# Kernel optimization log

Measured on AMD Instinct MI355X. Metric: run time of the kernel, lower is better.

## Reference

```python
import jax, jax.numpy as jnp
import numpy as np

N = 512          # nodes per sample (num_nodes)
B = 8            # batch size (samples)
H = 64           # hidden_dim
SPARSITY = 0.1
K = int(SPARSITY * N * (N - 1))  # edges kept per sample (fixed, static)


def setup_inputs() -> dict:
    key = jax.random.key(0)
    ks = jax.random.split(key, 8)

    def lin(k, fi, fo):
        w = jax.random.normal(k, (fi, fo), jnp.float32) / np.sqrt(fi).astype(np.float32)
        b = jnp.zeros((fo,), jnp.float32)
        return w, b

    w_emb, b_emb = lin(ks[0], 1, H)
    w_proj, b_proj = lin(ks[1], H, H)
    w1, b1 = lin(ks[2], 2 * H, H)
    w2, b2 = lin(ks[3], H, H // 2)
    w3, b3 = lin(ks[4], H // 2, 1)
    x = jax.random.uniform(ks[5], (B * N, 1), jnp.float32)  # abundances >= 0
    batch = jnp.repeat(jnp.arange(B, dtype=jnp.int32), N)   # [B*N]
    return dict(x=x, w_emb=w_emb, b_emb=b_emb, w_proj=w_proj, b_proj=b_proj,
                w1=w1, b1=b1, w2=w2, b2=b2, w3=w3, b3=b3, batch=batch)


def reference(x, w_emb, b_emb, w_proj, b_proj, w1, b1, w2, b2, w3, b3, batch):
    # node embedding + projection (dropout is eval-mode no-op)
    emb = jax.nn.relu(x @ w_emb + b_emb) @ w_proj + b_proj     # [B*N, H]
    emb = emb.reshape(B, N, H)
    # first pairwise-MLP layer: cat([e_i, e_j]) @ w1 == e_i @ w1a + e_j @ w1b
    w1a, w1b = w1[:H], w1[H:]
    ai = emb @ w1a                                            # [B, N, H]
    aj = emb @ w1b                                            # [B, N, H]
    h1 = jax.nn.relu(ai[:, :, None, :] + aj[:, None, :, :] + b1)   # [B, N, N, H]
    h2 = jax.nn.relu(jnp.einsum('bijh,hk->bijk', h1, w2) + b2)     # [B, N, N, H/2]
    probs = jax.nn.sigmoid(jnp.einsum('bijk,ko->bij', h2, w3) + b3[0])  # [B, N, N]
    probs = 0.5 * (probs + jnp.swapaxes(probs, 1, 2))          # symmetrize
    probs = probs * (1.0 - jnp.eye(N, dtype=probs.dtype))      # mask diagonal
    flat = probs.reshape(B, N * N)
    _, idx = jax.lax.top_k(flat, K)                            # [B, K]
    idx = jnp.sort(idx, axis=-1)                               # row-major order (dense_to_sparse)
    vals = jnp.take_along_axis(flat, idx, axis=-1)             # [B, K]
    offsets = (jnp.arange(B) * N)[:, None]                     # node offset per sample
    rows = idx // N + offsets
    cols = idx % N + offsets
    edge_index = jnp.stack([rows.reshape(-1), cols.reshape(-1)], axis=0)  # [2, B*K]
    edge_weights = vals.reshape(-1)                            # [B*K]
    adj = jnp.zeros((B, N * N), flat.dtype).at[jnp.arange(B)[:, None], idx].set(vals)
    adj = adj.reshape(B, N, N)                                 # sparse adjacency per sample
    return edge_index, edge_weights, adj
```

## Files before the change

kernel.cpp:

```cpp
#include <hip/hip_runtime.h>

#define NV 512
#define BV 8
#define HV 64
#define KSEL 26163
#define NNv (NV*NV)
#define BKv (BV*KSEL)

typedef unsigned int u32;
typedef __attribute__((ext_vector_type(2))) float f32x2;

__global__ void k_init(u32* __restrict__ hist4, u32* __restrict__ prefix,
                       u32* __restrict__ remK) {
    const int t = blockIdx.x * 256 + threadIdx.x;
    if (t < 8192) hist4[t] = 0u;
    if (t < 8) { prefix[t] = 0u; remK[t] = (u32)KSEL; }
}

__global__ void __launch_bounds__(256) k_embed(
    const float* __restrict__ x, const float* __restrict__ w_emb,
    const float* __restrict__ b_emb, const float* __restrict__ w_proj,
    const float* __restrict__ b_proj, const float* __restrict__ w1,
    float* __restrict__ ai, float* __restrict__ aj) {
    __shared__ float sh[4][64];
    __shared__ float se[4][64];
    const int c = threadIdx.x;
    const int lr = threadIdx.y;
    const int row = blockIdx.x * 4 + lr;
    const float xv = x[row];
    sh[lr][c] = fmaxf(fmaf(xv, w_emb[c], b_emb[c]), 0.f);
    __syncthreads();
    float e = 0.f;
#pragma unroll
    for (int h = 0; h < 64; ++h) e = fmaf(sh[lr][h], w_proj[h * 64 + c], e);
    se[lr][c] = e + b_proj[c];
    __syncthreads();
    float a0 = 0.f, a1 = 0.f;
#pragma unroll
    for (int h = 0; h < 64; ++h) {
        const float ev = se[lr][h];
        a0 = fmaf(ev, w1[h * 64 + c], a0);
        a1 = fmaf(ev, w1[(64 + h) * 64 + c], a1);
    }
    ai[row * 64 + c] = a0;
    aj[row * 64 + c] = a1;
}

#define F4(v, c) (((const float*)&(v))[c])
__global__ void __launch_bounds__(256, 2) k_pairs(
    const float* __restrict__ ai, const float* __restrict__ aj,
    const float* __restrict__ b1, const float* __restrict__ w2,
    const float* __restrict__ b2, const float* __restrict__ w3,
    const float* __restrict__ b3, float* __restrict__ probs) {
    __shared__ float s_ai[16 * 68];
    __shared__ float s_aj[64 * 68];
    __shared__ float s_b1[64];
    __shared__ float s_w2[64 * 32];
    __shared__ float s_b2[32];
    __shared__ float s_w3[32];
    __shared__ float s_b3v;
    const int tid = threadIdx.x;
    const int b  = blockIdx.z;
    const int i0 = blockIdx.y << 4;
    const int j0 = blockIdx.x << 6;

    {
        const int r  = tid >> 4;
        const int q4 = (tid & 15) << 2;
        *(float4*)&s_ai[r * 68 + q4] =
            *(const float4*)&ai[(((b << 9) + i0 + r) << 6) + q4];
#pragma unroll
        for (int s = 0; s < 4; ++s) {
            *(float4*)&s_aj[(r + 16 * s) * 68 + q4] =
                *(const float4*)&aj[(((b << 9) + j0 + 16 * s + r) << 6) + q4];
        }
        *(float4*)&s_w2[tid * 4]        = *(const float4*)&w2[tid * 4];
        *(float4*)&s_w2[1024 + tid * 4] = *(const float4*)&w2[1024 + tid * 4];
        if (tid < 64) s_b1[tid] = b1[tid];
        if (tid < 32) { s_b2[tid] = b2[tid]; s_w3[tid] = w3[tid]; }
        if (tid == 0) s_b3v = b3[0];
    }
    __syncthreads();

    const int tj = tid & 15;
    const int ti = tid >> 4;

    f32x2 acc0[16], acc1[16], acc2[16], acc3[16];
#pragma unroll
    for (int k = 0; k < 16; ++k) {
        acc0[k] = (f32x2){0.f, 0.f}; acc1[k] = (f32x2){0.f, 0.f};
        acc2[k] = (f32x2){0.f, 0.f}; acc3[k] = (f32x2){0.f, 0.f};
    }

#pragma unroll 1
    for (int h4 = 0; h4 < 64; h4 += 4) {
        const float4 aiv = *(const float4*)&s_ai[ti * 68 + h4];
        const float4 aj0 = *(const float4*)&s_aj[(tj     ) * 68 + h4];
        const float4 aj1 = *(const float4*)&s_aj[(tj + 16) * 68 + h4];
        const float4 aj2 = *(const float4*)&s_aj[(tj + 32) * 68 + h4];
        const float4 aj3 = *(const float4*)&s_aj[(tj + 48) * 68 + h4];
        const float4 b1v = *(const float4*)&s_b1[h4];
#pragma unroll
        for (int hh = 0; hh < 4; ++hh) {
            const float ah = F4(aiv, hh);
            const float bh = F4(b1v, hh);
            const float t0 = fmaxf((ah + F4(aj0, hh)) + bh, 0.f);
            const float t1 = fmaxf((ah + F4(aj1, hh)) + bh, 0.f);
            const float t2 = fmaxf((ah + F4(aj2, hh)) + bh, 0.f);
            const float t3 = fmaxf((ah + F4(aj3, hh)) + bh, 0.f);
            const f32x2 tt0 = {t0, t0};
            const f32x2 tt1 = {t1, t1};
            const f32x2 tt2 = {t2, t2};
            const f32x2 tt3 = {t3, t3};
            const float4* w4p = (const float4*)&s_w2[(h4 + hh) << 5];
            f32x2 w2r[16];
#pragma unroll
            for (int q = 0; q < 8; ++q) {
                const float4 w = w4p[q];
                w2r[2 * q]     = (f32x2){w.x, w.y};
                w2r[2 * q + 1] = (f32x2){w.z, w.w};
            }
#pragma unroll
            for (int k = 0; k < 16; ++k) {
                asm("v_pk_fma_f32 %0, %1, %2, %0" : "+v"(acc0[k]) : "v"(w2r[k]), "v"(tt0));
                asm("v_pk_fma_f32 %0, %1, %2, %0" : "+v"(acc1[k]) : "v"(w2r[k]), "v"(tt1));
                asm("v_pk_fma_f32 %0, %1, %2, %0" : "+v"(acc2[k]) : "v"(w2r[k]), "v"(tt2));
                asm("v_pk_fma_f32 %0, %1, %2, %0" : "+v"(acc3[k]) : "v"(w2r[k]), "v"(tt3));
            }
        }
    }

    float d0 = 0.f, d1 = 0.f, d2 = 0.f, d3 = 0.f;
#pragma unroll
    for (int k = 0; k < 32; ++k) {
        const float bk = s_b2[k], wk = s_w3[k];
        d0 = fmaf(fmaxf(acc0[k >> 1][k & 1] + bk, 0.f), wk, d0);
        d1 = fmaf(fmaxf(acc1[k >> 1][k & 1] + bk, 0.f), wk, d1);
        d2 = fmaf(fmaxf(acc2[k >> 1][k & 1] + bk, 0.f), wk, d2);
        d3 = fmaf(fmaxf(acc3[k >> 1][k & 1] + bk, 0.f), wk, d3);
    }
    const float bb = s_b3v;
    const float p0 = 1.f / (1.f + expf(-(d0 + bb)));
    const float p1 = 1.f / (1.f + expf(-(d1 + bb)));
    const float p2 = 1.f / (1.f + expf(-(d2 + bb)));
    const float p3 = 1.f / (1.f + expf(-(d3 + bb)));
    const int base = (((b << 9) + i0 + ti) << 9) + j0 + tj;
    probs[base]      = p0;
    probs[base + 16] = p1;
    probs[base + 32] = p2;
    probs[base + 48] = p3;
}

__global__ void k_sym(float* __restrict__ P) {
    const int b = blockIdx.y;
    int rem = blockIdx.x, ta = 0;
    while (rem >= 16 - ta) { rem -= 16 - ta; ++ta; }
    const int tb = ta + rem;
    const int r  = threadIdx.x >> 3;
    const int c4 = (threadIdx.x & 7) << 2;
    const int i = (ta << 5) + r;
    const int j = (tb << 5) + c4;
    float* Pb = P + b * NNv;
    float4 a = *(const float4*)&Pb[(i << 9) + j];
    float t0 = Pb[((j + 0) << 9) + i];
    float t1 = Pb[((j + 1) << 9) + i];
    float t2 = Pb[((j + 2) << 9) + i];
    float t3 = Pb[((j + 3) << 9) + i];
    __syncthreads();
    float4 o;
    o.x = (i == j + 0) ? 0.f : 0.5f * (a.x + t0);
    o.y = (i == j + 1) ? 0.f : 0.5f * (a.y + t1);
    o.z = (i == j + 2) ? 0.f : 0.5f * (a.z + t2);
    o.w = (i == j + 3) ? 0.f : 0.5f * (a.w + t3);
    *(float4*)&Pb[(i << 9) + j] = o;
    Pb[((j + 0) << 9) + i] = o.x;
    Pb[((j + 1) << 9) + i] = o.y;
    Pb[((j + 2) << 9) + i] = o.z;
    Pb[((j + 3) << 9) + i] = o.w;
}

template <int P>
__global__ void k_hist(const float* __restrict__ probs,
                       const u32* __restrict__ prefix, u32* __restrict__ hist) {
    __shared__ u32 lh[1024];
    const int t = threadIdx.x;
    lh[t] = 0u; lh[256 + t] = 0u; lh[512 + t] = 0u; lh[768 + t] = 0u;
    __syncthreads();
    const int b = blockIdx.y;
    u32 pref = 0u;
    if constexpr (P > 0) pref = prefix[b];
    const float* Pb = probs + b * NNv;
    const int base = blockIdx.x * 4096 + t;
    const int rep = (t & 3) << 8;
#pragma unroll
    for (int e = 0; e < 16; ++e) {
        const u32 key = __float_as_uint(Pb[base + e * 256]);
        bool ok = true;
        if constexpr (P > 0) ok = ((key >> (32 - 8 * P)) == pref);
        if (ok) atomicAdd(&lh[rep + ((key >> (24 - 8 * P)) & 255u)], 1u);
    }
    __syncthreads();
    const u32 sum = lh[t] + lh[256 + t] + lh[512 + t] + lh[768 + t];
    if (sum) atomicAdd(&hist[b * 256 + t], sum);
}

__global__ void k_sel(const u32* __restrict__ hist, u32* __restrict__ prefix,
                      u32* __restrict__ remK) {
    __shared__ u32 s[256];
    __shared__ int cstar;
    const int b = blockIdx.x, t = threadIdx.x;
    const u32 h = hist[b * 256 + t];
    s[t] = h;
    if (t == 0) cstar = 0;
    __syncthreads();
    for (int off = 1; off < 256; off <<= 1) {
        const u32 v = (t + off < 256) ? s[t + off] : 0u;
        __syncthreads();
        s[t] += v;
        __syncthreads();
    }
    const u32 rem = remK[b];
    if (s[t] >= rem) atomicMax(&cstar, t);
    __syncthreads();
    if (t == cstar) {
        const u32 above = (t < 255) ? s[t + 1] : 0u;
        remK[b] = rem - above;
        prefix[b] = (prefix[b] << 8) | (u32)t;
    }
}

__global__ void k_count(const float* __restrict__ P, const u32* __restrict__ Tk,
                        u32* __restrict__ bgt, u32* __restrict__ beq) {
    __shared__ u32 sg[256], se[256];
    const int b = blockIdx.y, blk = blockIdx.x, t = threadIdx.x;
    const u32 T = Tk[b];
    const float4 v = *(const float4*)&P[b * NNv + blk * 1024 + t * 4];
    const u32 k0 = __float_as_uint(v.x), k1 = __float_as_uint(v.y);
    const u32 k2 = __float_as_uint(v.z), k3 = __float_as_uint(v.w);
    sg[t] = (u32)(k0 > T) + (k1 > T) + (k2 > T) + (k3 > T);
    se[t] = (u32)(k0 == T) + (k1 == T) + (k2 == T) + (k3 == T);
    __syncthreads();
    for (int s = 128; s > 0; s >>= 1) {
        if (t < s) { sg[t] += sg[t + s]; se[t] += se[t + s]; }
        __syncthreads();
    }
    if (t == 0) { bgt[b * 256 + blk] = sg[0]; beq[b * 256 + blk] = se[0]; }
}

__global__ void k_scan(const u32* __restrict__ bgt, const u32* __restrict__ beq,
                       u32* __restrict__ goff, u32* __restrict__ eoff) {
    __shared__ u32 sg[256], se[256];
    const int b = blockIdx.x, t = threadIdx.x;
    const u32 g = bgt[b * 256 + t], e = beq[b * 256 + t];
    sg[t] = g; se[t] = e;
    __syncthreads();
    for (int off = 1; off < 256; off <<= 1) {
        const u32 ag = (t >= off) ? sg[t - off] : 0u;
        const u32 ae = (t >= off) ? se[t - off] : 0u;
        __syncthreads();
        sg[t] += ag; se[t] += ae;
        __syncthreads();
    }
    goff[b * 256 + t] = sg[t] - g;
    eoff[b * 256 + t] = se[t] - e;
}

__global__ void k_write(const float* __restrict__ P, const u32* __restrict__ Tk,
                        const u32* __restrict__ Rk, const u32* __restrict__ goff,
                        const u32* __restrict__ eoff, float* __restrict__ out) {
    __shared__ u32 sg[256], se[256];
    const int b = blockIdx.y, blk = blockIdx.x, t = threadIdx.x;
    const u32 T = Tk[b];
    const u32 R = Rk[b];
    const int pbase = b * NNv;
    const int fi0 = blk * 1024 + t * 4;
    const float4 v = *(const float4*)&P[pbase + fi0];
    float vv[4] = {v.x, v.y, v.z, v.w};
    u32 kk[4];
#pragma unroll
    for (int q = 0; q < 4; ++q) kk[q] = __float_as_uint(vv[q]);
    u32 gt = 0, eq = 0;
#pragma unroll
    for (int q = 0; q < 4; ++q) { gt += (kk[q] > T); eq += (kk[q] == T); }
    sg[t] = gt; se[t] = eq;
    __syncthreads();
    for (int off = 1; off < 256; off <<= 1) {
        const u32 ag = (t >= off) ? sg[t - off] : 0u;
        const u32 ae = (t >= off) ? se[t - off] : 0u;
        __syncthreads();
        sg[t] += ag; se[t] += ae;
        __syncthreads();
    }
    u32 gt_before = goff[b * 256 + blk] + sg[t] - gt;
    u32 eq_before = eoff[b * 256 + blk] + se[t] - eq;
#pragma unroll
    for (int q = 0; q < 4; ++q) {
        const u32 key = kk[q];
        const float val = vv[q];
        const bool selg = key > T;
        const bool sele = (key == T) && (eq_before < R);
        if (selg || sele) {
            const u32 ties = (eq_before < R) ? eq_before : R;
            const u32 pos = selg ? (gt_before + ties) : (gt_before + eq_before);
            const int g = b * KSEL + (int)pos;
            const int fi = fi0 + q;
            const int row = fi >> 9, col = fi & 511;
            out[g]            = (float)(row + (b << 9));
            out[BKv + g]      = (float)(col + (b << 9));
            out[2 * BKv + g]  = val;
            out[3 * BKv + pbase + fi] = val;
        }
        gt_before += (u32)selg;
        eq_before += (u32)(key == T);
    }
}

extern "C" void kernel_launch(void* const* d_in, const int* in_sizes, int n_in,
                              void* d_out, int out_size, void* d_ws, size_t ws_size,
                              hipStream_t stream) {
    const float* x      = (const float*)d_in[0];
    const float* w_emb  = (const float*)d_in[1];
    const float* b_emb  = (const float*)d_in[2];
    const float* w_proj = (const float*)d_in[3];
    const float* b_proj = (const float*)d_in[4];
    const float* w1     = (const float*)d_in[5];
    const float* b1     = (const float*)d_in[6];
    const float* w2     = (const float*)d_in[7];
    const float* b2     = (const float*)d_in[8];
    const float* w3     = (const float*)d_in[9];
    const float* b3     = (const float*)d_in[10];
    (void)in_sizes; (void)n_in; (void)ws_size;

    char* ws = (char*)d_ws;
    float* ai    = (float*)(ws);
    float* aj    = (float*)(ws + 1048576);
    float* probs = (float*)(ws + 2097152);
    u32* hist4  = (u32*)(ws + 10485760);
    u32* prefix = (u32*)(ws + 10518528);
    u32* remK   = (u32*)(ws + 10518560);
    u32* bgt    = (u32*)(ws + 10518592);
    u32* beq    = (u32*)(ws + 10526784);
    u32* goff   = (u32*)(ws + 10534976);
    u32* eoff   = (u32*)(ws + 10543168);

    float* out = (float*)d_out;

    hipMemsetAsync(d_out, 0, (size_t)out_size * sizeof(float), stream);
    k_init<<<32, 256, 0, stream>>>(hist4, prefix, remK);
    k_embed<<<1024, dim3(64, 4, 1), 0, stream>>>(x, w_emb, b_emb, w_proj, b_proj, w1, ai, aj);
    k_pairs<<<dim3(8, 32, 8), 256, 0, stream>>>(ai, aj, b1, w2, b2, w3, b3, probs);
    k_sym<<<dim3(136, 8), 256, 0, stream>>>(probs);
    k_hist<0><<<dim3(64, 8), 256, 0, stream>>>(probs, prefix, hist4);
    k_sel<<<8, 256, 0, stream>>>(hist4, prefix, remK);
    k_hist<1><<<dim3(64, 8), 256, 0, stream>>>(probs, prefix, hist4 + 2048);
    k_sel<<<8, 256, 0, stream>>>(hist4 + 2048, prefix, remK);
    k_hist<2><<<dim3(64, 8), 256, 0, stream>>>(probs, prefix, hist4 + 4096);
    k_sel<<<8, 256, 0, stream>>>(hist4 + 4096, prefix, remK);
    k_hist<3><<<dim3(64, 8), 256, 0, stream>>>(probs, prefix, hist4 + 6144);
    k_sel<<<8, 256, 0, stream>>>(hist4 + 6144, prefix, remK);
    k_count<<<dim3(256, 8), 256, 0, stream>>>(probs, prefix, bgt, beq);
    k_scan<<<8, 256, 0, stream>>>(bgt, beq, goff, eoff);
    k_write<<<dim3(256, 8), 256, 0, stream>>>(probs, prefix, remK, goff, eoff, out);
}
```

Before: 170.9 us.

## Compute pairwise MLP with split-fp16 MFMA and exact-recompute threshold band

After: 203.1 us. 18.8% more time.

```diff
diff --git a/kernel.cpp b/kernel.cpp
--- a/kernel.cpp
+++ b/kernel.cpp
@@ -2,26 +2,22 @@
 
 #define NV 512
 #define BV 8
-#define HV 64
 #define KSEL 26163
 #define NNv (NV*NV)
 #define BKv (BV*KSEL)
+#define CAPB 32768
+#define DELTA 1e-4f
 
 typedef unsigned int u32;
-typedef __attribute__((ext_vector_type(2))) float f32x2;
-
-__global__ void k_init(u32* __restrict__ hist4, u32* __restrict__ prefix,
-                       u32* __restrict__ remK) {
-    const int t = blockIdx.x * 256 + threadIdx.x;
-    if (t < 8192) hist4[t] = 0u;
-    if (t < 8) { prefix[t] = 0u; remK[t] = (u32)KSEL; }
-}
+typedef __attribute__((ext_vector_type(8))) _Float16 f16x8;
+typedef __attribute__((ext_vector_type(4))) float f32x4;
 
 __global__ void __launch_bounds__(256) k_embed(
     const float* __restrict__ x, const float* __restrict__ w_emb,
     const float* __restrict__ b_emb, const float* __restrict__ w_proj,
     const float* __restrict__ b_proj, const float* __restrict__ w1,
-    float* __restrict__ ai, float* __restrict__ aj) {
+    const float* __restrict__ b1,
+    float* __restrict__ ai, float* __restrict__ aj, float* __restrict__ ajb) {
     __shared__ float sh[4][64];
     __shared__ float se[4][64];
     const int c = threadIdx.x;
@@ -44,111 +40,109 @@
     }
     ai[row * 64 + c] = a0;
     aj[row * 64 + c] = a1;
-}
-
-#define F4(v, c) (((const float*)&(v))[c])
-__global__ void __launch_bounds__(256, 2) k_pairs(
-    const float* __restrict__ ai, const float* __restrict__ aj,
-    const float* __restrict__ b1, const float* __restrict__ w2,
-    const float* __restrict__ b2, const float* __restrict__ w3,
-    const float* __restrict__ b3, float* __restrict__ probs) {
-    __shared__ float s_ai[16 * 68];
-    __shared__ float s_aj[64 * 68];
-    __shared__ float s_b1[64];
-    __shared__ float s_w2[64 * 32];
-    __shared__ float s_b2[32];
-    __shared__ float s_w3[32];
-    __shared__ float s_b3v;
+    ajb[row * 64 + c] = a1 + b1[c];
+}
+
+__global__ void __launch_bounds__(256) k_pairs_mfma(
+    const float* __restrict__ ai, const float* __restrict__ ajb,
+    const float* __restrict__ w2, const float* __restrict__ b2,
+    const float* __restrict__ w3, const float* __restrict__ b3,
+    float* __restrict__ probs) {
+    __shared__ float s_ai[2048];
     const int tid = threadIdx.x;
-    const int b  = blockIdx.z;
-    const int i0 = blockIdx.y << 4;
+    const int b = blockIdx.z;
+    const int i0 = blockIdx.y << 5;
     const int j0 = blockIdx.x << 6;
-
     {
-        const int r  = tid >> 4;
-        const int q4 = (tid & 15) << 2;
-        *(float4*)&s_ai[r * 68 + q4] =
-            *(const float4*)&ai[(((b << 9) + i0 + r) << 6) + q4];
-#pragma unroll
-        for (int s = 0; s < 4; ++s) {
-            *(float4*)&s_aj[(r + 16 * s) * 68 + q4] =
-                *(const float4*)&aj[(((b << 9) + j0 + 16 * s + r) << 6) + q4];
-        }
-        *(float4*)&s_w2[tid * 4]        = *(const float4*)&w2[tid * 4];
-        *(float4*)&s_w2[1024 + tid * 4] = *(const float4*)&w2[1024 + tid * 4];
-        if (tid < 64) s_b1[tid] = b1[tid];
-        if (tid < 32) { s_b2[tid] = b2[tid]; s_w3[tid] = w3[tid]; }
-        if (tid == 0) s_b3v = b3[0];
-    }
-    __syncthreads();
-
-    const int tj = tid & 15;
-    const int ti = tid >> 4;
-
-    f32x2 acc0[16], acc1[16], acc2[16], acc3[16];
-#pragma unroll
-    for (int k = 0; k < 16; ++k) {
-        acc0[k] = (f32x2){0.f, 0.f}; acc1[k] = (f32x2){0.f, 0.f};
-        acc2[k] = (f32x2){0.f, 0.f}; acc3[k] = (f32x2){0.f, 0.f};
-    }
-
-#pragma unroll 1
-    for (int h4 = 0; h4 < 64; h4 += 4) {
-        const float4 aiv = *(const float4*)&s_ai[ti * 68 + h4];
-        const float4 aj0 = *(const float4*)&s_aj[(tj     ) * 68 + h4];
-        const float4 aj1 = *(const float4*)&s_aj[(tj + 16) * 68 + h4];
-        const float4 aj2 = *(const float4*)&s_aj[(tj + 32) * 68 + h4];
-        const float4 aj3 = *(const float4*)&s_aj[(tj + 48) * 68 + h4];
-        const float4 b1v = *(const float4*)&s_b1[h4];
-#pragma unroll
-        for (int hh = 0; hh < 4; ++hh) {
-            const float ah = F4(aiv, hh);
-            const float bh = F4(b1v, hh);
-            const float t0 = fmaxf((ah + F4(aj0, hh)) + bh, 0.f);
-            const float t1 = fmaxf((ah + F4(aj1, hh)) + bh, 0.f);
-            const float t2 = fmaxf((ah + F4(aj2, hh)) + bh, 0.f);
-            const float t3 = fmaxf((ah + F4(aj3, hh)) + bh, 0.f);
-            const f32x2 tt0 = {t0, t0};
-            const f32x2 tt1 = {t1, t1};
-            const f32x2 tt2 = {t2, t2};
-            const f32x2 tt3 = {t3, t3};
-            const float4* w4p = (const float4*)&s_w2[(h4 + hh) << 5];
-            f32x2 w2r[16];
-#pragma unroll
-            for (int q = 0; q < 8; ++q) {
-                const float4 w = w4p[q];
-                w2r[2 * q]     = (f32x2){w.x, w.y};
-                w2r[2 * q + 1] = (f32x2){w.z, w.w};
+        const int r = tid >> 3, c8 = (tid & 7) << 3;
+        const float* src = &ai[(((b << 9) + i0 + r) << 6) + c8];
+        *(float4*)&s_ai[(r << 6) + c8]     = *(const float4*)&src[0];
+        *(float4*)&s_ai[(r << 6) + c8 + 4] = *(const float4*)&src[4];
+    }
+    const int lane = tid & 63;
+    const int wv = tid >> 6;
+    const int lp = lane & 15;
+    const int lg = lane >> 4;
+    const int j = j0 + (wv << 4) + lp;
+
+    float ajr[2][8];
+    {
+        const float* base = &ajb[(((b << 9) + j) << 6) + (lg << 3)];
+        *(float4*)&ajr[0][0] = *(const float4*)&base[0];
+        *(float4*)&ajr[0][4] = *(const float4*)&base[4];
+        *(float4*)&ajr[1][0] = *(const float4*)&base[32];
+        *(float4*)&ajr[1][4] = *(const float4*)&base[36];
+    }
+    f16x8 Ah[2][2], Al[2][2];
+#pragma unroll
+    for (int kt = 0; kt < 2; ++kt)
+#pragma unroll
+        for (int ch = 0; ch < 2; ++ch)
+#pragma unroll
+            for (int e = 0; e < 8; ++e) {
+                const float wv2 = w2[((ch << 5) + (lg << 3) + e) * 32 + (kt << 4) + lp];
+                const _Float16 wh = (_Float16)wv2;
+                Ah[kt][ch][e] = wh;
+                Al[kt][ch][e] = (_Float16)((wv2 - (float)wh) * 2048.0f);
             }
-#pragma unroll
-            for (int k = 0; k < 16; ++k) {
-                asm("v_pk_fma_f32 %0, %1, %2, %0" : "+v"(acc0[k]) : "v"(w2r[k]), "v"(tt0));
-                asm("v_pk_fma_f32 %0, %1, %2, %0" : "+v"(acc1[k]) : "v"(w2r[k]), "v"(tt1));
-                asm("v_pk_fma_f32 %0, %1, %2, %0" : "+v"(acc2[k]) : "v"(w2r[k]), "v"(tt2));
-                asm("v_pk_fma_f32 %0, %1, %2, %0" : "+v"(acc3[k]) : "v"(w2r[k]), "v"(tt3));
-            }
-        }
-    }
-
-    float d0 = 0.f, d1 = 0.f, d2 = 0.f, d3 = 0.f;
-#pragma unroll
-    for (int k = 0; k < 32; ++k) {
-        const float bk = s_b2[k], wk = s_w3[k];
-        d0 = fmaf(fmaxf(acc0[k >> 1][k & 1] + bk, 0.f), wk, d0);
-        d1 = fmaf(fmaxf(acc1[k >> 1][k & 1] + bk, 0.f), wk, d1);
-        d2 = fmaf(fmaxf(acc2[k >> 1][k & 1] + bk, 0.f), wk, d2);
-        d3 = fmaf(fmaxf(acc3[k >> 1][k & 1] + bk, 0.f), wk, d3);
-    }
-    const float bb = s_b3v;
-    const float p0 = 1.f / (1.f + expf(-(d0 + bb)));
-    const float p1 = 1.f / (1.f + expf(-(d1 + bb)));
-    const float p2 = 1.f / (1.f + expf(-(d2 + bb)));
-    const float p3 = 1.f / (1.f + expf(-(d3 + bb)));
-    const int base = (((b << 9) + i0 + ti) << 9) + j0 + tj;
-    probs[base]      = p0;
-    probs[base + 16] = p1;
-    probs[base + 32] = p2;
-    probs[base + 48] = p3;
+    float b2r[2][4], w3r[2][4];
+#pragma unroll
+    for (int kt = 0; kt < 2; ++kt)
+#pragma unroll
+        for (int r = 0; r < 4; ++r) {
+            b2r[kt][r] = b2[(kt << 4) + (lg << 2) + r];
+            w3r[kt][r] = w3[(kt << 4) + (lg << 2) + r];
+        }
+    const float b3v = b3[0];
+    __syncthreads();
+
+    for (int i = 0; i < 32; ++i) {
+        float ar[2][8];
+        const float* arow = &s_ai[(i << 6) + (lg << 3)];
+        *(float4*)&ar[0][0] = *(const float4*)&arow[0];
+        *(float4*)&ar[0][4] = *(const float4*)&arow[4];
+        *(float4*)&ar[1][0] = *(const float4*)&arow[32];
+        *(float4*)&ar[1][4] = *(const float4*)&arow[36];
+        f16x8 Bh0, Bh1, Bl0, Bl1;
+#pragma unroll
+        for (int e = 0; e < 8; ++e) {
+            const float t0 = fmaxf(ar[0][e] + ajr[0][e], 0.f) * 256.0f;
+            const float t1 = fmaxf(ar[1][e] + ajr[1][e], 0.f) * 256.0f;
+            const _Float16 h0 = (_Float16)t0;
+            const _Float16 h1 = (_Float16)t1;
+            Bh0[e] = h0; Bl0[e] = (_Float16)((t0 - (float)h0) * 2048.0f);
+            Bh1[e] = h1; Bl1[e] = (_Float16)((t1 - (float)h1) * 2048.0f);
+        }
+        f32x4 am0 = {0.f,0.f,0.f,0.f}, am1 = {0.f,0.f,0.f,0.f};
+        f32x4 ac0 = {0.f,0.f,0.f,0.f}, ac1 = {0.f,0.f,0.f,0.f};
+        am0 = __builtin_amdgcn_mfma_f32_16x16x32_f16(Ah[0][0], Bh0, am0, 0, 0, 0);
+        am0 = __builtin_amdgcn_mfma_f32_16x16x32_f16(Ah[0][1], Bh1, am0, 0, 0, 0);
+        ac0 = __builtin_amdgcn_mfma_f32_16x16x32_f16(Ah[0][0], Bl0, ac0, 0, 0, 0);
+        ac0 = __builtin_amdgcn_mfma_f32_16x16x32_f16(Ah[0][1], Bl1, ac0, 0, 0, 0);
+        ac0 = __builtin_amdgcn_mfma_f32_16x16x32_f16(Al[0][0], Bh0, ac0, 0, 0, 0);
+        ac0 = __builtin_amdgcn_mfma_f32_16x16x32_f16(Al[0][1], Bh1, ac0, 0, 0, 0);
+        am1 = __builtin_amdgcn_mfma_f32_16x16x32_f16(Ah[1][0], Bh0, am1, 0, 0, 0);
+        am1 = __builtin_amdgcn_mfma_f32_16x16x32_f16(Ah[1][1], Bh1, am1, 0, 0, 0);
+        ac1 = __builtin_amdgcn_mfma_f32_16x16x32_f16(Ah[1][0], Bl0, ac1, 0, 0, 0);
+        ac1 = __builtin_amdgcn_mfma_f32_16x16x32_f16(Ah[1][1], Bl1, ac1, 0, 0, 0);
+        ac1 = __builtin_amdgcn_mfma_f32_16x16x32_f16(Al[1][0], Bh0, ac1, 0, 0, 0);
+        ac1 = __builtin_amdgcn_mfma_f32_16x16x32_f16(Al[1][1], Bh1, ac1, 0, 0, 0);
+        float s = 0.f;
+#pragma unroll
+        for (int r = 0; r < 4; ++r) {
+            const float h2 = fmaf(ac0[r], 1.9073486328125e-6f, am0[r] * 0.00390625f);
+            s = fmaf(fmaxf(h2 + b2r[0][r], 0.f), w3r[0][r], s);
+        }
+#pragma unroll
+        for (int r = 0; r < 4; ++r) {
+            const float h2 = fmaf(ac1[r], 1.9073486328125e-6f, am1[r] * 0.00390625f);
+            s = fmaf(fmaxf(h2 + b2r[1][r], 0.f), w3r[1][r], s);
+        }
+        s += __shfl_xor(s, 16);
+        s += __shfl_xor(s, 32);
+        const float p = 1.f / (1.f + expf(-(s + b3v)));
+        if (lane < 16) probs[(((b << 9) + i0 + i) << 9) + j] = p;
+    }
 }
 
 __global__ void k_sym(float* __restrict__ P) {
@@ -179,7 +173,7 @@
     Pb[((j + 3) << 9) + i] = o.w;
 }
 
-template <int P>
+template <int PASS>
 __global__ void k_hist(const float* __restrict__ probs,
                        const u32* __restrict__ prefix, u32* __restrict__ hist) {
     __shared__ u32 lh[1024];
@@ -188,7 +182,7 @@
     __syncthreads();
     const int b = blockIdx.y;
     u32 pref = 0u;
-    if constexpr (P > 0) pref = prefix[b];
+    if constexpr (PASS > 0) pref = prefix[b];
     const float* Pb = probs + b * NNv;
     const int base = blockIdx.x * 4096 + t;
     const int rep = (t & 3) << 8;
@@ -196,22 +190,20 @@
     for (int e = 0; e < 16; ++e) {
         const u32 key = __float_as_uint(Pb[base + e * 256]);
         bool ok = true;
-        if constexpr (P > 0) ok = ((key >> (32 - 8 * P)) == pref);
-        if (ok) atomicAdd(&lh[rep + ((key >> (24 - 8 * P)) & 255u)], 1u);
+        if constexpr (PASS > 0) ok = ((key >> (32 - 8 * PASS)) == pref);
+        if (ok) atomicAdd(&lh[rep + ((key >> (24 - 8 * PASS)) & 255u)], 1u);
     }
     __syncthreads();
     const u32 sum = lh[t] + lh[256 + t] + lh[512 + t] + lh[768 + t];
     if (sum) atomicAdd(&hist[b * 256 + t], sum);
 }
 
-__global__ void k_sel(const u32* __restrict__ hist, u32* __restrict__ prefix,
-                      u32* __restrict__ remK) {
+template <int FIRST>
+__global__ void k_selp(const u32* __restrict__ hist, u32* __restrict__ prefix,
+                       u32* __restrict__ rem) {
     __shared__ u32 s[256];
-    __shared__ int cstar;
     const int b = blockIdx.x, t = threadIdx.x;
-    const u32 h = hist[b * 256 + t];
-    s[t] = h;
-    if (t == 0) cstar = 0;
+    s[t] = hist[b * 256 + t];
     __syncthreads();
     for (int off = 1; off < 256; off <<= 1) {
         const u32 v = (t + off < 256) ? s[t + off] : 0u;
@@ -219,99 +211,252 @@
         s[t] += v;
         __syncthreads();
     }
-    const u32 rem = remK[b];
-    if (s[t] >= rem) atomicMax(&cstar, t);
-    __syncthreads();
-    if (t == cstar) {
-        const u32 above = (t < 255) ? s[t + 1] : 0u;
-        remK[b] = rem - above;
+    const u32 remv = FIRST ? (u32)KSEL : rem[b];
+    const u32 above = (t < 255) ? s[t + 1] : 0u;
+    if (s[t] >= remv && above < remv) {
+        rem[b] = remv - above;
         prefix[b] = (prefix[b] << 8) | (u32)t;
     }
 }
 
-__global__ void k_count(const float* __restrict__ P, const u32* __restrict__ Tk,
-                        u32* __restrict__ bgt, u32* __restrict__ beq) {
-    __shared__ u32 sg[256], se[256];
+__global__ void k_thr(const u32* __restrict__ prefix, float* __restrict__ thr) {
+    const int b = threadIdx.x;
+    if (b >= 8) return;
+    const u32 p24 = prefix[b];
+    thr[b]     = __uint_as_float(p24 << 8) - 2.f * DELTA;
+    thr[8 + b] = __uint_as_float((p24 + 1u) << 8) + 2.f * DELTA;
+}
+
+__global__ void __launch_bounds__(256) k_band(
+    const float* __restrict__ P, const float* __restrict__ thr,
+    u32* __restrict__ C_in, u32* __restrict__ bandCnt, u32* __restrict__ bandIdx) {
+    __shared__ u32 lidx[1024];
+    __shared__ u32 lcnt, lhi, gbase;
     const int b = blockIdx.y, blk = blockIdx.x, t = threadIdx.x;
-    const u32 T = Tk[b];
-    const float4 v = *(const float4*)&P[b * NNv + blk * 1024 + t * 4];
-    const u32 k0 = __float_as_uint(v.x), k1 = __float_as_uint(v.y);
-    const u32 k2 = __float_as_uint(v.z), k3 = __float_as_uint(v.w);
-    sg[t] = (u32)(k0 > T) + (k1 > T) + (k2 > T) + (k3 > T);
-    se[t] = (u32)(k0 == T) + (k1 == T) + (k2 == T) + (k3 == T);
-    __syncthreads();
-    for (int s = 128; s > 0; s >>= 1) {
-        if (t < s) { sg[t] += sg[t + s]; se[t] += se[t + s]; }
+    if (t == 0) { lcnt = 0u; lhi = 0u; }
+    __syncthreads();
+    const float Tlo = thr[b], Thi = thr[8 + b];
+    const int fi0 = blk * 1024 + t * 4;
+    const float4 v = *(const float4*)&P[b * NNv + fi0];
+    const float vv[4] = {v.x, v.y, v.z, v.w};
+    u32 hc = 0;
+#pragma unroll
+    for (int q = 0; q < 4; ++q) {
+        const float xq = vv[q];
+        if (xq > Thi) ++hc;
+        else if (xq >= Tlo) { u32 p = atomicAdd(&lcnt, 1u); lidx[p] = (u32)(fi0 + q); }
+    }
+    if (hc) atomicAdd(&lhi, hc);
+    __syncthreads();
+    if (t == 0) {
+        if (lhi) atomicAdd(&C_in[b], lhi);
+        gbase = lcnt ? atomicAdd(&bandCnt[b], lcnt) : 0u;
+    }
+    __syncthreads();
+    for (u32 p = t; p < lcnt; p += 256) {
+        const u32 g = gbase + p;
+        if (g < (u32)CAPB) bandIdx[b * CAPB + g] = lidx[p];
+    }
+}
+
+__device__ __forceinline__ float exact_p(const float* __restrict__ rai,
+                                         const float* __restrict__ raj,
+                                         const float* __restrict__ s_w2,
+                                         const float* __restrict__ s_b1,
+                                         const float* __restrict__ s_b2,
+                                         const float* __restrict__ s_w3,
+                                         float b3v) {
+    float acc[32];
+#pragma unroll
+    for (int k = 0; k < 32; ++k) acc[k] = 0.f;
+#pragma unroll 1
+    for (int h0 = 0; h0 < 64; h0 += 16) {
+        float A[16], J[16];
+#pragma unroll
+        for (int q = 0; q < 4; ++q) {
+            *(float4*)&A[q * 4] = *(const float4*)&rai[h0 + q * 4];
+            *(float4*)&J[q * 4] = *(const float4*)&raj[h0 + q * 4];
+        }
+#pragma unroll
+        for (int hh = 0; hh < 16; ++hh) {
+            const float tv = fmaxf((A[hh] + J[hh]) + s_b1[h0 + hh], 0.f);
+#pragma unroll
+            for (int k = 0; k < 32; ++k) acc[k] = fmaf(tv, s_w2[(h0 + hh) * 32 + k], acc[k]);
+        }
+    }
+    float d = 0.f;
+#pragma unroll
+    for (int k = 0; k < 32; ++k) d = fmaf(fmaxf(acc[k] + s_b2[k], 0.f), s_w3[k], d);
+    return 1.f / (1.f + expf(-(d + b3v)));
+}
+
+__global__ void __launch_bounds__(256) k_band_exact(
+    const float* __restrict__ ai, const float* __restrict__ aj,
+    const float* __restrict__ b1, const float* __restrict__ w2,
+    const float* __restrict__ b2, const float* __restrict__ w3,
+    const float* __restrict__ b3, const u32* __restrict__ bandCnt,
+    const u32* __restrict__ bandIdx, float* __restrict__ bandVal) {
+    __shared__ float s_w2[2048];
+    __shared__ float s_b1[64], s_b2[32], s_w3[32];
+    const int b = blockIdx.y, t = threadIdx.x;
+    {
+        const int o = t * 8;
+        *(float4*)&s_w2[o]     = *(const float4*)&w2[o];
+        *(float4*)&s_w2[o + 4] = *(const float4*)&w2[o + 4];
+        if (t < 64) s_b1[t] = b1[t];
+        if (t < 32) { s_b2[t] = b2[t]; s_w3[t] = w3[t]; }
+    }
+    __syncthreads();
+    const u32 nb = min(bandCnt[b], (u32)CAPB);
+    const float b3v = b3[0];
+    for (u32 e = blockIdx.x * 256 + t; e < nb; e += 2048) {
+        const u32 idx = bandIdx[b * CAPB + e];
+        const int i = (int)(idx >> 9), j = (int)(idx & 511u);
+        const float* ri  = &ai[(((b << 9) + i)) << 6];
+        const float* rj  = &aj[(((b << 9) + j)) << 6];
+        const float* rj2 = &ai[(((b << 9) + j)) << 6];
+        const float* ri2 = &aj[(((b << 9) + i)) << 6];
+        const float p1 = exact_p(ri, rj, s_w2, s_b1, s_b2, s_w3, b3v);
+        const float p2 = exact_p(rj2, ri2, s_w2, s_b1, s_b2, s_w3, b3v);
+        bandVal[b * CAPB + e] = 0.5f * (p1 + p2);
+    }
+}
+
+__global__ void __launch_bounds__(256) k_band_select(
+    const u32* __restrict__ bandCnt, const u32* __restrict__ C_in,
+    const u32* __restrict__ bandIdx, const float* __restrict__ bandVal,
+    u32* __restrict__ bitmap) {
+    __shared__ u32 red[256];
+    __shared__ u32 tie[8192];
+    __shared__ u32 tieCnt;
+    const int b = blockIdx.x, t = threadIdx.x;
+    const u32 nb = min(bandCnt[b], (u32)CAPB);
+    const u32 Kp = (u32)KSEL - C_in[b];
+    const u32* vb = (const u32*)(bandVal + b * CAPB);
+    const u32* ib = bandIdx + b * CAPB;
+    u32* bm = bitmap + b * 8192;
+    u32 mn = 0xFFFFFFFFu, mx = 0u;
+    for (u32 e = t; e < nb; e += 256) { const u32 v = vb[e]; mn = min(mn, v); mx = max(mx, v); }
+    red[t] = mn; __syncthreads();
+    for (int s = 128; s > 0; s >>= 1) { if (t < s) red[t] = min(red[t], red[t + s]); __syncthreads(); }
+    const u32 glo = red[0]; __syncthreads();
+    red[t] = mx; __syncthreads();
+    for (int s = 128; s > 0; s >>= 1) { if (t < s) red[t] = max(red[t], red[t + s]); __syncthreads(); }
+    const u32 ghi = red[0]; __syncthreads();
+    u32 lo = glo, hi = ghi;
+    while (lo < hi) {
+        const u32 mid = lo + ((hi - lo) >> 1);
+        u32 c = 0;
+        for (u32 e = t; e < nb; e += 256) c += (vb[e] > mid);
+        red[t] = c; __syncthreads();
+        for (int s = 128; s > 0; s >>= 1) { if (t < s) red[t] += red[t + s]; __syncthreads(); }
+        const u32 tot = red[0]; __syncthreads();
+        if (tot >= Kp) lo = mid + 1; else hi = mid;
+    }
+    const u32 Tx = lo;
+    if (t == 0) tieCnt = 0u;
+    __syncthreads();
+    u32 c = 0;
+    for (u32 e = t; e < nb; e += 256) {
+        const u32 v = vb[e];
+        if (v > Tx) {
+            ++c;
+            const u32 idx = ib[e];
+            atomicOr(&bm[idx >> 5], 1u << (idx & 31u));
+        } else if (v == Tx) {
+            const u32 p = atomicAdd(&tieCnt, 1u);
+            if (p < 8192u) tie[p] = ib[e];
+        }
+    }
+    red[t] = c; __syncthreads();
+    for (int s = 128; s > 0; s >>= 1) { if (t < s) red[t] += red[t + s]; __syncthreads(); }
+    const u32 Ap = red[0]; __syncthreads();
+    const u32 Rp = Kp - Ap;
+    const u32 E = min(tieCnt, 8192u);
+    for (u32 e = t; e < E; e += 256) {
+        const u32 my = tie[e];
+        u32 r = 0;
+        for (u32 m = 0; m < E; ++m) r += (tie[m] < my);
+        if (r < Rp) atomicOr(&bm[my >> 5], 1u << (my & 31u));
+    }
+}
+
+__global__ void k_count(const float* __restrict__ P, const float* __restrict__ thr,
+                        const u32* __restrict__ bitmap, u32* __restrict__ bgt) {
+    __shared__ u32 sg[256];
+    const int b = blockIdx.y, blk = blockIdx.x, t = threadIdx.x;
+    const float Thi = thr[8 + b];
+    const int fi0 = blk * 1024 + t * 4;
+    const float4 v = *(const float4*)&P[b * NNv + fi0];
+    const float vv[4] = {v.x, v.y, v.z, v.w};
+    const u32 w = bitmap[b * 8192 + (fi0 >> 5)];
+    const u32 sh = (u32)(fi0 & 31);
+    u32 cnt = 0;
+#pragma unroll
+    for (int q = 0; q < 4; ++q) cnt += (vv[q] > Thi) || ((w >> (sh + q)) & 1u);
+    sg[t] = cnt;
+    __syncthreads();
+    for (int s = 128; s > 0; s >>= 1) { if (t < s) sg[t] += sg[t + s]; __syncthreads(); }
+    if (t == 0) bgt[b * 256 + blk] = sg[0];
+}
+
+__global__ void k_scan1(const u32* __restrict__ bgt, u32* __restrict__ goff) {
+    __shared__ u32 sg[256];
+    const int b = blockIdx.x, t = threadIdx.x;
+    const u32 g = bgt[b * 256 + t];
+    sg[t] = g;
+    __syncthreads();
+    for (int off = 1; off < 256; off <<= 1) {
+        const u32 a = (t >= off) ? sg[t - off] : 0u;
         __syncthreads();
-    }
-    if (t == 0) { bgt[b * 256 + blk] = sg[0]; beq[b * 256 + blk] = se[0]; }
-}
-
-__global__ void k_scan(const u32* __restrict__ bgt, const u32* __restrict__ beq,
-                       u32* __restrict__ goff, u32* __restrict__ eoff) {
-    __shared__ u32 sg[256], se[256];
-    const int b = blockIdx.x, t = threadIdx.x;
-    const u32 g = bgt[b * 256 + t], e = beq[b * 256 + t];
-    sg[t] = g; se[t] = e;
-    __syncthreads();
-    for (int off = 1; off < 256; off <<= 1) {
-        const u32 ag = (t >= off) ? sg[t - off] : 0u;
-        const u32 ae = (t >= off) ? se[t - off] : 0u;
+        sg[t] += a;
         __syncthreads();
-        sg[t] += ag; se[t] += ae;
-        __syncthreads();
     }
     goff[b * 256 + t] = sg[t] - g;
-    eoff[b * 256 + t] = se[t] - e;
-}
-
-__global__ void k_write(const float* __restrict__ P, const u32* __restrict__ Tk,
-                        const u32* __restrict__ Rk, const u32* __restrict__ goff,
-                        const u32* __restrict__ eoff, float* __restrict__ out) {
-    __shared__ u32 sg[256], se[256];
+}
+
+__global__ void k_write(const float* __restrict__ P, const float* __restrict__ thr,
+                        const u32* __restrict__ bitmap, const u32* __restrict__ goff,
+                        float* __restrict__ out) {
+    __shared__ u32 sg[256];
     const int b = blockIdx.y, blk = blockIdx.x, t = threadIdx.x;
-    const u32 T = Tk[b];
-    const u32 R = Rk[b];
+    const float Thi = thr[8 + b];
     const int pbase = b * NNv;
     const int fi0 = blk * 1024 + t * 4;
     const float4 v = *(const float4*)&P[pbase + fi0];
-    float vv[4] = {v.x, v.y, v.z, v.w};
-    u32 kk[4];
-#pragma unroll
-    for (int q = 0; q < 4; ++q) kk[q] = __float_as_uint(vv[q]);
-    u32 gt = 0, eq = 0;
-#pragma unroll
-    for (int q = 0; q < 4; ++q) { gt += (kk[q] > T); eq += (kk[q] == T); }
-    sg[t] = gt; se[t] = eq;
+    const float vv[4] = {v.x, v.y, v.z, v.w};
+    const u32 w = bitmap[b * 8192 + (fi0 >> 5)];
+    const u32 sh = (u32)(fi0 & 31);
+    bool sel[4];
+    u32 cnt = 0;
+#pragma unroll
+    for (int q = 0; q < 4; ++q) {
+        sel[q] = (vv[q] > Thi) || ((w >> (sh + q)) & 1u);
+        cnt += sel[q];
+    }
+    sg[t] = cnt;
     __syncthreads();
     for (int off = 1; off < 256; off <<= 1) {
-        const u32 ag = (t >= off) ? sg[t - off] : 0u;
-        const u32 ae = (t >= off) ? se[t - off] : 0u;
+        const u32 a = (t >= off) ? sg[t - off] : 0u;
         __syncthreads();
-        sg[t] += ag; se[t] += ae;
+        sg[t] += a;
         __syncthreads();
     }
-    u32 gt_before = goff[b * 256 + blk] + sg[t] - gt;
-    u32 eq_before = eoff[b * 256 + blk] + se[t] - eq;
+    u32 pos = goff[b * 256 + blk] + sg[t] - cnt;
 #pragma unroll
     for (int q = 0; q < 4; ++q) {
-        const u32 key = kk[q];
-        const float val = vv[q];
-        const bool selg = key > T;
-        const bool sele = (key == T) && (eq_before < R);
-        if (selg || sele) {
-            const u32 ties = (eq_before < R) ? eq_before : R;
-            const u32 pos = selg ? (gt_before + ties) : (gt_before + eq_before);
-            const int g = b * KSEL + (int)pos;
-            const int fi = fi0 + q;
-            const int row = fi >> 9, col = fi & 511;
-            out[g]            = (float)(row + (b << 9));
-            out[BKv + g]      = (float)(col + (b << 9));
-            out[2 * BKv + g]  = val;
-            out[3 * BKv + pbase + fi] = val;
-        }
-        gt_before += (u32)selg;
-        eq_before += (u32)(key == T);
+        if (sel[q]) {
+            if (pos < (u32)KSEL) {
+                const int g = b * KSEL + (int)pos;
+                const int fi = fi0 + q;
+                const int row = fi >> 9, col = fi & 511;
+                out[g]           = (float)(row + (b << 9));
+                out[BKv + g]     = (float)(col + (b << 9));
+                out[2 * BKv + g] = vv[q];
+                out[3 * BKv + pbase + fi] = vv[q];
+            }
+            ++pos;
+        }
     }
 }
 
@@ -332,33 +477,44 @@
     (void)in_sizes; (void)n_in; (void)ws_size;
 
     char* ws = (char*)d_ws;
-    float* ai    = (float*)(ws);
-    float* aj    = (float*)(ws + 1048576);
-    float* probs = (float*)(ws + 2097152);
-    u32* hist4  = (u32*)(ws + 10485760);
-    u32* prefix = (u32*)(ws + 10518528);
-    u32* remK   = (u32*)(ws + 10518560);
-    u32* bgt    = (u32*)(ws + 10518592);
-    u32* beq    = (u32*)(ws + 10526784);
-    u32* goff   = (u32*)(ws + 10534976);
-    u32* eoff   = (u32*)(ws + 10543168);
+    float* ai      = (float*)(ws);
+    float* aj      = (float*)(ws + 1048576);
+    float* ajb     = (float*)(ws + 2097152);
+    float* probs   = (float*)(ws + 3145728);
+    u32*   bandIdx = (u32*)  (ws + 11534336);
+    float* bandVal = (float*)(ws + 12582912);
+    const size_t SOFF = 13631488;
+    u32*   hist0   = (u32*)  (ws + SOFF);
+    u32*   hist1   = (u32*)  (ws + SOFF + 8192);
+    u32*   hist2   = (u32*)  (ws + SOFF + 16384);
+    u32*   prefix  = (u32*)  (ws + SOFF + 24576);
+    u32*   rem     = (u32*)  (ws + SOFF + 24608);
+    float* thr     = (float*)(ws + SOFF + 24640);
+    u32*   C_in    = (u32*)  (ws + SOFF + 24704);
+    u32*   bandCnt = (u32*)  (ws + SOFF + 24736);
+    u32*   bitmap  = (u32*)  (ws + SOFF + 24832);
+    u32*   bgt     = (u32*)  (ws + SOFF + 286976);
+    u32*   goff    = (u32*)  (ws + SOFF + 295168);
 
     float* out = (float*)d_out;
 
     hipMemsetAsync(d_out, 0, (size_t)out_size * sizeof(float), stream);
-    k_init<<<32, 256, 0, stream>>>(hist4, prefix, remK);
-    k_embed<<<1024, dim3(64, 4, 1), 0, stream>>>(x, w_emb, b_emb, w_proj, b_proj, w1, ai, aj);
-    k_pairs<<<dim3(8, 32, 8), 256, 0, stream>>>(ai, aj, b1, w2, b2, w3, b3, probs);
+    hipMemsetAsync(ws + SOFF, 0, 286976, stream);
+
+    k_embed<<<1024, dim3(64, 4, 1), 0, stream>>>(x, w_emb, b_emb, w_proj, b_proj, w1, b1, ai, aj, ajb);
+    k_pairs_mfma<<<dim3(8, 16, 8), 256, 0, stream>>>(ai, ajb, w2, b2, w3, b3, probs);
     k_sym<<<dim3(136, 8), 256, 0, stream>>>(probs);
-    k_hist<0><<<dim3(64, 8), 256, 0, stream>>>(probs, prefix, hist4);
-    k_sel<<<8, 256, 0, stream>>>(hist4, prefix, remK);
-    k_hist<1><<<dim3(64, 8), 256, 0, stream>>>(probs, prefix, hist4 + 2048);
-    k_sel<<<8, 256, 0, stream>>>(hist4 + 2048, prefix, remK);
-    k_hist<2><<<dim3(64, 8), 256, 0, stream>>>(probs, prefix, hist4 + 4096);
-    k_sel<<<8, 256, 0, stream>>>(hist4 + 4096, prefix, remK);
-    k_hist<3><<<dim3(64, 8), 256, 0, stream>>>(probs, prefix, hist4 + 6144);
-    k_sel<<<8, 256, 0, stream>>>(hist4 + 6144, prefix, remK);
-    k_count<<<dim3(256, 8), 256, 0, stream>>>(probs, prefix, bgt, beq);
-    k_scan<<<8, 256, 0, stream>>>(bgt, beq, goff, eoff);
-    k_write<<<dim3(256, 8), 256, 0, stream>>>(probs, prefix, remK, goff, eoff, out);
-}
+    k_hist<0><<<dim3(64, 8), 256, 0, stream>>>(probs, prefix, hist0);
+    k_selp<1><<<8, 256, 0, stream>>>(hist0, prefix, rem);
+    k_hist<1><<<dim3(64, 8), 256, 0, stream>>>(probs, prefix, hist1);
+    k_selp<0><<<8, 256, 0, stream>>>(hist1, prefix, rem);
+    k_hist<2><<<dim3(64, 8), 256, 0, stream>>>(probs, prefix, hist2);
+    k_selp<0><<<8, 256, 0, stream>>>(hist2, prefix, rem);
+    k_thr<<<1, 64, 0, stream>>>(prefix, thr);
+    k_band<<<dim3(256, 8), 256, 0, stream>>>(probs, thr, C_in, bandCnt, bandIdx);
+    k_band_exact<<<dim3(8, 8), 256, 0, stream>>>(ai, aj, b1, w2, b2, w3, b3, bandCnt, bandIdx, bandVal);
+    k_band_select<<<8, 256, 0, stream>>>(bandCnt, C_in, bandIdx, bandVal, bitmap);
+    k_count<<<dim3(256, 8), 256, 0, stream>>>(probs, thr, bitmap, bgt);
+    k_scan1<<<8, 256, 0, stream>>>(bgt, goff);
+    k_write<<<dim3(256, 8), 256, 0, stream>>>(probs, thr, bitmap, goff, out);
+}
```
